# Optimization experiments

Measured on AMD Instinct MI355X. Metric: run time of the kernel, lower is better.

Reference implementation:

```python
import jax, jax.numpy as jnp
import numpy as np

N, DIN, DOUT = 8192, 256, 128
NEG_SLOPE = 0.01         # F.leaky_relu default
MASK_VAL = -9.0e15       # from the torch source


def setup_inputs() -> dict:
    key = jax.random.key(0)
    kx, kadj, kW, kbW, ka1, ka2, kba = jax.random.split(key, 7)
    x = jax.random.normal(kx, (N, DIN), dtype=jnp.float32)
    adj = jax.random.randint(kadj, (N, N), 0, 2, dtype=jnp.int32)
    # Linear W: input_dim -> output_dim
    W = jax.random.normal(kW, (DIN, DOUT), dtype=jnp.float32) * (1.0 / np.sqrt(DIN))
    bW = jax.random.normal(kbW, (DOUT,), dtype=jnp.float32) * 0.01
    # Linear a: 2*output_dim -> 1, split into the h_i part (a1) and h_j part (a2)
    a1 = jax.random.normal(ka1, (DOUT,), dtype=jnp.float32) * (1.0 / np.sqrt(2 * DOUT))
    a2 = jax.random.normal(ka2, (DOUT,), dtype=jnp.float32) * (1.0 / np.sqrt(2 * DOUT))
    ba = jax.random.normal(kba, (), dtype=jnp.float32) * 0.01
    return {"x": x, "adj": adj, "W": W, "bW": bW, "a1": a1, "a2": a2, "ba": ba}


def reference(x, adj, W, bW, a1, a2, ba):
    # h = W x + b  -> [N, DOUT]
    h = x @ W + bW
    # e[i,j] = leaky_relu(a . [h_i, h_j] + ba) = leaky_relu(a1.h_i + a2.h_j + ba)
    s_src = h @ a1            # [N]
    s_dst = h @ a2            # [N]
    e = s_src[:, None] + s_dst[None, :] + ba   # [N, N]
    e = jnp.where(e > 0, e, NEG_SLOPE * e)
    # mask non-edges, row softmax over neighbors j
    e = jnp.where(adj > 0, e, MASK_VAL)
    alpha = jax.nn.softmax(e, axis=1)          # [N, N]
    # dropout is identity in eval mode (dropout_rate=0)
    return alpha @ h                            # [N, DOUT]
```

## Files before the change

### kernel.cpp

```cpp
#include <hip/hip_runtime.h>
#include <hip/hip_bf16.h>


#define NN 8192
#define DIN 256
#define DOUT 128

typedef __attribute__((ext_vector_type(8))) short short8;
typedef __attribute__((ext_vector_type(4))) float floatx4;

__global__ void prep_wt(const float* __restrict__ W, __hip_bfloat16* __restrict__ WT) {
    int e = blockIdx.x * blockDim.x + threadIdx.x;
    if (e < DIN * DOUT) {
        int k = e >> 7;
        int d = e & 127;
        WT[d * DIN + k] = __float2bfloat16(W[e]);
    }
}

__global__ __launch_bounds__(256, 4) void gat_h(
    const float* __restrict__ x, const __hip_bfloat16* __restrict__ WT,
    const float* __restrict__ bW, const float* __restrict__ a1, const float* __restrict__ a2,
    __hip_bfloat16* __restrict__ hbT, float* __restrict__ s_src, float* __restrict__ s_dst) {
    int tid = threadIdx.x;
    int w = tid >> 6, lane = tid & 63;
    int lm = lane & 15, lq = lane >> 4;
    int i0 = blockIdx.x * 32;
    int r0 = (w >> 1) * 16;
    int c0 = (w & 1) * 64;

    __shared__ float s1s[32], s2s[32];
    if (tid < 32) { s1s[tid] = 0.f; s2s[tid] = 0.f; }
    __syncthreads();

    floatx4 acc[4] = {};
#pragma unroll
    for (int kk = 0; kk < DIN; kk += 32) {
        const float4* xp = (const float4*)&x[(size_t)(i0 + r0 + lm) * DIN + kk + lq * 8];
        float4 xa = xp[0], xb = xp[1];
        union { short8 v; __hip_bfloat16 h[8]; } af;
        af.h[0] = __float2bfloat16(xa.x); af.h[1] = __float2bfloat16(xa.y);
        af.h[2] = __float2bfloat16(xa.z); af.h[3] = __float2bfloat16(xa.w);
        af.h[4] = __float2bfloat16(xb.x); af.h[5] = __float2bfloat16(xb.y);
        af.h[6] = __float2bfloat16(xb.z); af.h[7] = __float2bfloat16(xb.w);
#pragma unroll
        for (int t = 0; t < 4; t++) {
            int d = c0 + 16 * t + lm;
            short8 bf = *(const short8*)&WT[(size_t)d * DIN + kk + lq * 8];
            acc[t] = __builtin_amdgcn_mfma_f32_16x16x32_bf16(af.v, bf, acc[t], 0, 0, 0);
        }
    }
    float s1[4] = {0.f, 0.f, 0.f, 0.f}, s2[4] = {0.f, 0.f, 0.f, 0.f};
#pragma unroll
    for (int t = 0; t < 4; t++) {
        int d = c0 + 16 * t + lm;
        float A1 = a1[d], A2 = a2[d], B = bW[d];
#pragma unroll
        for (int r = 0; r < 4; r++) {
            int row = r0 + lq * 4 + r;
            float h = acc[t][r] + B;
            hbT[(size_t)d * NN + i0 + row] = __float2bfloat16(h);
            s1[r] += h * A1;
            s2[r] += h * A2;
        }
    }
#pragma unroll
    for (int r = 0; r < 4; r++) {
        for (int m = 1; m < 16; m <<= 1) {
            s1[r] += __shfl_xor(s1[r], m, 64);
            s2[r] += __shfl_xor(s2[r], m, 64);
        }
    }
    if (lm == 0) {
#pragma unroll
        for (int r = 0; r < 4; r++) {
            int row = r0 + lq * 4 + r;
            atomicAdd(&s1s[row], s1[r]);
            atomicAdd(&s2s[row], s2[r]);
        }
    }
    __syncthreads();
    if (tid < 32) {
        s_src[i0 + tid] = s1s[tid];
        s_dst[i0 + tid] = s2s[tid];
    }
}

__global__ __launch_bounds__(256, 4) void gat_attn(
    const int* __restrict__ adj, const float* __restrict__ s_src,
    const float* __restrict__ s_dst, const float* __restrict__ ba_p,
    const __hip_bfloat16* __restrict__ hbT,
    float* __restrict__ num, float* __restrict__ lpart) {
    int tid = threadIdx.x;
    int b = blockIdx.x;
    int ib = b & 511;
    int jh = b >> 9;
    int i0 = ib * 16;
    size_t jbase = (size_t)jh * 4096;

    __shared__ float ss[16];
    __shared__ __hip_bfloat16 pb[2][16][32];

    if (tid < 16) ss[tid] = s_src[i0 + tid];
    float ba = ba_p[0];
    __syncthreads();

    int w = tid >> 6, lane = tid & 63;
    int lm = lane & 15, lq = lane >> 4;
    int pi = tid >> 4;
    int pj = (tid & 15) * 2;

    floatx4 acc0 = {}, acc1 = {};
    float lsum = 0.f;
    float ssi = ss[pi] + ba;

    const int* adjrow = adj + (size_t)(i0 + pi) * NN + jbase + pj;
    const float* sdrow = s_dst + jbase + pj;
    const __hip_bfloat16* hb0p = hbT + (size_t)(w * 32 + lm) * NN + jbase + lq * 8;
    const __hip_bfloat16* hb1p = hb0p + (size_t)16 * NN;

    int2 adjn = *(const int2*)adjrow;
    float2 sdn = *(const float2*)sdrow;
    short8 hb0n = *(const short8*)hb0p;
    short8 hb1n = *(const short8*)hb1p;

    for (int t = 0; t < 128; t++) {
        int2 adjc = adjn;
        float2 sdc = sdn;
        short8 hb0 = hb0n, hb1 = hb1n;
        if (t < 127) {
            adjn = *(const int2*)(adjrow + (t + 1) * 32);
            sdn = *(const float2*)(sdrow + (t + 1) * 32);
            hb0n = *(const short8*)(hb0p + (t + 1) * 32);
            hb1n = *(const short8*)(hb1p + (t + 1) * 32);
        }
        float e0 = ssi + sdc.x; e0 = e0 > 0.f ? e0 : 0.01f * e0;
        float e1 = ssi + sdc.y; e1 = e1 > 0.f ? e1 : 0.01f * e1;
        float p0 = adjc.x ? __expf(e0) : 0.f;
        float p1 = adjc.y ? __expf(e1) : 0.f;
        __hip_bfloat16 q0 = __float2bfloat16(p0), q1 = __float2bfloat16(p1);
        lsum += __bfloat162float(q0) + __bfloat162float(q1);
        int buf = t & 1;
        pb[buf][pi][pj] = q0;
        pb[buf][pi][pj + 1] = q1;
        __syncthreads();
        short8 af = *(const short8*)&pb[buf][lm][lq * 8];
        acc0 = __builtin_amdgcn_mfma_f32_16x16x32_bf16(af, hb0, acc0, 0, 0, 0);
        acc1 = __builtin_amdgcn_mfma_f32_16x16x32_bf16(af, hb1, acc1, 0, 0, 0);
    }
    for (int m = 1; m < 16; m <<= 1) lsum += __shfl_xor(lsum, m, 64);
    if ((tid & 15) == 0) lpart[(size_t)jh * NN + i0 + pi] = lsum;

    float* nb = num + (size_t)jh * NN * DOUT;
#pragma unroll
    for (int r = 0; r < 4; r++) {
        int row = i0 + lq * 4 + r;
        nb[(size_t)row * DOUT + w * 32 + lm] = acc0[r];
        nb[(size_t)row * DOUT + w * 32 + 16 + lm] = acc1[r];
    }
}

__global__ void gat_combine(const float* __restrict__ num, const float* __restrict__ lpart,
                            float* __restrict__ out) {
    int gid = blockIdx.x * blockDim.x + threadIdx.x;
    int idx = gid * 4;
    int i = idx >> 7;
    float inv = 1.0f / (lpart[i] + lpart[NN + i]);
    float4 n0 = *(const float4*)&num[idx];
    float4 n1 = *(const float4*)&num[(size_t)NN * DOUT + idx];
    float4 o;
    o.x = (n0.x + n1.x) * inv;
    o.y = (n0.y + n1.y) * inv;
    o.z = (n0.z + n1.z) * inv;
    o.w = (n0.w + n1.w) * inv;
    *(float4*)&out[idx] = o;
}

extern "C" void kernel_launch(void* const* d_in, const int* in_sizes, int n_in,
                              void* d_out, int out_size, void* d_ws, size_t ws_size,
                              hipStream_t stream) {
    const float* x  = (const float*)d_in[0];
    const int* adj  = (const int*)d_in[1];
    const float* W  = (const float*)d_in[2];
    const float* bW = (const float*)d_in[3];
    const float* a1 = (const float*)d_in[4];
    const float* a2 = (const float*)d_in[5];
    const float* ba = (const float*)d_in[6];
    float* out = (float*)d_out;

    char* ws = (char*)d_ws;
    __hip_bfloat16* hbT = (__hip_bfloat16*)ws;
    __hip_bfloat16* WT  = (__hip_bfloat16*)(ws + 2097152);
    float* s_src        = (float*)(ws + 2162688);
    float* s_dst        = (float*)(ws + 2195456);
    float* num          = (float*)(ws + 2228224);
    float* lpart        = (float*)(ws + 10616832);

    prep_wt<<<128, 256, 0, stream>>>(W, WT);
    gat_h<<<256, 256, 0, stream>>>(x, WT, bW, a1, a2, hbT, s_src, s_dst);
    gat_attn<<<1024, 256, 0, stream>>>(adj, s_src, s_dst, ba, hbT, num, lpart);
    gat_combine<<<1024, 256, 0, stream>>>(num, lpart, out);
}
```

Measured before the change: 514.9 us.

## Restructure attention kernel: per-wave row tiles, full DOUT per wave, no LDS sync

Each wave now owns 16 rows and computes all 128 output columns, building its bf16 probability fragment directly in registers. This removes the shared-memory staging and the per-iteration __syncthreads, and the row sums come from an MFMA against a ones vector. The j-dimension split is chosen from the workspace size (up to 8), which adds parallelism but also more partial-sum traffic in the combine pass. Every wave re-reads the hbT rows independently, with wider adj loads of 8 ints per lane.

```diff
diff --git a/kernel.cpp b/kernel.cpp
--- a/kernel.cpp
+++ b/kernel.cpp
@@ -90,89 +90,94 @@
     const int* __restrict__ adj, const float* __restrict__ s_src,
     const float* __restrict__ s_dst, const float* __restrict__ ba_p,
     const __hip_bfloat16* __restrict__ hbT,
-    float* __restrict__ num, float* __restrict__ lpart) {
+    float* __restrict__ num, float* __restrict__ lpart, int njt) {
     int tid = threadIdx.x;
-    int b = blockIdx.x;
-    int ib = b & 511;
-    int jh = b >> 9;
-    int i0 = ib * 16;
-    size_t jbase = (size_t)jh * 4096;
-
-    __shared__ float ss[16];
-    __shared__ __hip_bfloat16 pb[2][16][32];
-
-    if (tid < 16) ss[tid] = s_src[i0 + tid];
-    float ba = ba_p[0];
-    __syncthreads();
-
     int w = tid >> 6, lane = tid & 63;
     int lm = lane & 15, lq = lane >> 4;
-    int pi = tid >> 4;
-    int pj = (tid & 15) * 2;
-
-    floatx4 acc0 = {}, acc1 = {};
-    float lsum = 0.f;
-    float ssi = ss[pi] + ba;
-
-    const int* adjrow = adj + (size_t)(i0 + pi) * NN + jbase + pj;
-    const float* sdrow = s_dst + jbase + pj;
-    const __hip_bfloat16* hb0p = hbT + (size_t)(w * 32 + lm) * NN + jbase + lq * 8;
-    const __hip_bfloat16* hb1p = hb0p + (size_t)16 * NN;
-
-    int2 adjn = *(const int2*)adjrow;
-    float2 sdn = *(const float2*)sdrow;
-    short8 hb0n = *(const short8*)hb0p;
-    short8 hb1n = *(const short8*)hb1p;
-
-    for (int t = 0; t < 128; t++) {
-        int2 adjc = adjn;
-        float2 sdc = sdn;
-        short8 hb0 = hb0n, hb1 = hb1n;
-        if (t < 127) {
-            adjn = *(const int2*)(adjrow + (t + 1) * 32);
-            sdn = *(const float2*)(sdrow + (t + 1) * 32);
-            hb0n = *(const short8*)(hb0p + (t + 1) * 32);
-            hb1n = *(const short8*)(hb1p + (t + 1) * 32);
-        }
-        float e0 = ssi + sdc.x; e0 = e0 > 0.f ? e0 : 0.01f * e0;
-        float e1 = ssi + sdc.y; e1 = e1 > 0.f ? e1 : 0.01f * e1;
-        float p0 = adjc.x ? __expf(e0) : 0.f;
-        float p1 = adjc.y ? __expf(e1) : 0.f;
-        __hip_bfloat16 q0 = __float2bfloat16(p0), q1 = __float2bfloat16(p1);
-        lsum += __bfloat162float(q0) + __bfloat162float(q1);
-        int buf = t & 1;
-        pb[buf][pi][pj] = q0;
-        pb[buf][pi][pj + 1] = q1;
-        __syncthreads();
-        short8 af = *(const short8*)&pb[buf][lm][lq * 8];
-        acc0 = __builtin_amdgcn_mfma_f32_16x16x32_bf16(af, hb0, acc0, 0, 0, 0);
-        acc1 = __builtin_amdgcn_mfma_f32_16x16x32_bf16(af, hb1, acc1, 0, 0, 0);
-    }
-    for (int m = 1; m < 16; m <<= 1) lsum += __shfl_xor(lsum, m, 64);
-    if ((tid & 15) == 0) lpart[(size_t)jh * NN + i0 + pi] = lsum;
-
-    float* nb = num + (size_t)jh * NN * DOUT;
-#pragma unroll
-    for (int r = 0; r < 4; r++) {
-        int row = i0 + lq * 4 + r;
-        nb[(size_t)row * DOUT + w * 32 + lm] = acc0[r];
-        nb[(size_t)row * DOUT + w * 32 + 16 + lm] = acc1[r];
+    int b = blockIdx.x;
+    int ib = b & 127;
+    int jh = b >> 7;
+    int i0 = ib * 64 + w * 16;
+    int jb0 = jh * (njt * 32);
+
+    float ssi = s_src[i0 + lm] + ba_p[0];
+
+    const int* arow = adj + (size_t)(i0 + lm) * NN + jb0 + lq * 8;
+    const float* sd = s_dst + jb0 + lq * 8;
+    const __hip_bfloat16* hbb = hbT + (size_t)lm * NN + jb0 + lq * 8;
+
+    floatx4 acc[8] = {};
+    floatx4 accd = {};
+    const short8 ones = { 0x3F80, 0x3F80, 0x3F80, 0x3F80, 0x3F80, 0x3F80, 0x3F80, 0x3F80 };
+
+    int4 a0 = *(const int4*)arow;
+    int4 a1 = *(const int4*)(arow + 4);
+    float4 d0 = *(const float4*)sd;
+    float4 d1 = *(const float4*)(sd + 4);
+
+    for (int t = 0; t < njt; t++) {
+        int4 ca0 = a0, ca1 = a1;
+        float4 cd0 = d0, cd1 = d1;
+        if (t + 1 < njt) {
+            a0 = *(const int4*)(arow + (t + 1) * 32);
+            a1 = *(const int4*)(arow + (t + 1) * 32 + 4);
+            d0 = *(const float4*)(sd + (t + 1) * 32);
+            d1 = *(const float4*)(sd + (t + 1) * 32 + 4);
+        }
+        float p[8];
+        {
+            float e;
+            e = ssi + cd0.x; e = fmaxf(e, 0.01f * e); p[0] = ca0.x ? __expf(e) : 0.f;
+            e = ssi + cd0.y; e = fmaxf(e, 0.01f * e); p[1] = ca0.y ? __expf(e) : 0.f;
+            e = ssi + cd0.z; e = fmaxf(e, 0.01f * e); p[2] = ca0.z ? __expf(e) : 0.f;
+            e = ssi + cd0.w; e = fmaxf(e, 0.01f * e); p[3] = ca0.w ? __expf(e) : 0.f;
+            e = ssi + cd1.x; e = fmaxf(e, 0.01f * e); p[4] = ca1.x ? __expf(e) : 0.f;
+            e = ssi + cd1.y; e = fmaxf(e, 0.01f * e); p[5] = ca1.y ? __expf(e) : 0.f;
+            e = ssi + cd1.z; e = fmaxf(e, 0.01f * e); p[6] = ca1.z ? __expf(e) : 0.f;
+            e = ssi + cd1.w; e = fmaxf(e, 0.01f * e); p[7] = ca1.w ? __expf(e) : 0.f;
+        }
+        union { short8 v; __hip_bfloat162 q[4]; } af;
+        af.q[0] = __float22bfloat162_rn(make_float2(p[0], p[1]));
+        af.q[1] = __float22bfloat162_rn(make_float2(p[2], p[3]));
+        af.q[2] = __float22bfloat162_rn(make_float2(p[4], p[5]));
+        af.q[3] = __float22bfloat162_rn(make_float2(p[6], p[7]));
+
+        size_t off = (size_t)t * 32;
+#pragma unroll
+        for (int f = 0; f < 8; f++) {
+            short8 bf = *(const short8*)(hbb + (size_t)f * 16 * NN + off);
+            acc[f] = __builtin_amdgcn_mfma_f32_16x16x32_bf16(af.v, bf, acc[f], 0, 0, 0);
+        }
+        accd = __builtin_amdgcn_mfma_f32_16x16x32_bf16(af.v, ones, accd, 0, 0, 0);
+    }
+
+    float* nb = num + ((size_t)jh * NN + i0) * DOUT;
+#pragma unroll
+    for (int f = 0; f < 8; f++)
+#pragma unroll
+        for (int r = 0; r < 4; r++)
+            nb[(size_t)(lq * 4 + r) * DOUT + f * 16 + lm] = acc[f][r];
+    if (lm == 0) {
+#pragma unroll
+        for (int r = 0; r < 4; r++)
+            lpart[(size_t)jh * NN + i0 + lq * 4 + r] = accd[r];
     }
 }
 
 __global__ void gat_combine(const float* __restrict__ num, const float* __restrict__ lpart,
-                            float* __restrict__ out) {
+                            float* __restrict__ out, int jsplit) {
     int gid = blockIdx.x * blockDim.x + threadIdx.x;
     int idx = gid * 4;
     int i = idx >> 7;
-    float inv = 1.0f / (lpart[i] + lpart[NN + i]);
-    float4 n0 = *(const float4*)&num[idx];
-    float4 n1 = *(const float4*)&num[(size_t)NN * DOUT + idx];
-    float4 o;
-    o.x = (n0.x + n1.x) * inv;
-    o.y = (n0.y + n1.y) * inv;
-    o.z = (n0.z + n1.z) * inv;
-    o.w = (n0.w + n1.w) * inv;
+    float den = 0.f;
+    for (int s = 0; s < jsplit; s++) den += lpart[(size_t)s * NN + i];
+    float inv = 1.0f / den;
+    float4 o = make_float4(0.f, 0.f, 0.f, 0.f);
+    for (int s = 0; s < jsplit; s++) {
+        float4 n = *(const float4*)&num[(size_t)s * NN * DOUT + idx];
+        o.x += n.x; o.y += n.y; o.z += n.z; o.w += n.w;
+    }
+    o.x *= inv; o.y *= inv; o.z *= inv; o.w *= inv;
     *(float4*)&out[idx] = o;
 }
 
@@ -193,11 +198,17 @@
     __hip_bfloat16* WT  = (__hip_bfloat16*)(ws + 2097152);
     float* s_src        = (float*)(ws + 2162688);
     float* s_dst        = (float*)(ws + 2195456);
-    float* num          = (float*)(ws + 2228224);
-    float* lpart        = (float*)(ws + 10616832);
+    float* lpart        = (float*)(ws + 2228224);
+    float* num          = (float*)(ws + 2490368);
+
+    size_t base = 2490368;
+    int jsplit = 2;
+    if (ws_size >= base + (size_t)8 * NN * DOUT * 4) jsplit = 8;
+    else if (ws_size >= base + (size_t)4 * NN * DOUT * 4) jsplit = 4;
+    int njt = NN / (32 * jsplit);
 
     prep_wt<<<128, 256, 0, stream>>>(W, WT);
     gat_h<<<256, 256, 0, stream>>>(x, WT, bW, a1, a2, hbT, s_src, s_dst);
-    gat_attn<<<1024, 256, 0, stream>>>(adj, s_src, s_dst, ba, hbT, num, lpart);
-    gat_combine<<<1024, 256, 0, stream>>>(num, lpart, out);
-}
+    gat_attn<<<128 * jsplit, 256, 0, stream>>>(adj, s_src, s_dst, ba, hbT, num, lpart, njt);
+    gat_combine<<<1024, 256, 0, stream>>>(num, lpart, out, jsplit);
+}
```

After: 512.3 us. No clear change (-0.5%).
